# Kernel tuning notes

Measured on AMD Instinct MI355X. Metric: run time of the kernel, lower is better.

## Reference

```python
import jax, jax.numpy as jnp
import numpy as np

N, G, E, R = 32768, 2048, 1146880, 3
NIN, GIN, F, OUT = 6, 4, 64, 1


def _w(k, fan_in, fan_out):
    return (jax.random.normal(k, (fan_in, fan_out), jnp.float32) / np.sqrt(fan_in)).astype(jnp.float32)


def setup_inputs() -> dict:
    key = jax.random.key(0)
    ks = jax.random.split(key, 20)
    x = jax.random.normal(ks[0], (N, NIN), jnp.float32)
    u = jax.random.normal(ks[1], (G, GIN), jnp.float32)
    batch = jnp.sort(jax.random.randint(ks[2], (N,), 0, G))
    hyperedge_index = jax.random.randint(ks[3], (R, E), 0, N)
    batch_hyper = jnp.sort(jax.random.randint(ks[4], (E,), 0, G))
    inp = {
        "x": x, "u": u, "batch": batch,
        "hyperedge_index": hyperedge_index, "batch_hyper": batch_hyper, "r": R,
        # mlp_x: (NIN+GIN)->F->F->F
        "W1": _w(ks[5], NIN + GIN, F), "b1": jnp.zeros((F,), jnp.float32),
        "W2": _w(ks[6], F, F), "b2": jnp.zeros((F,), jnp.float32),
        "W3": _w(ks[7], F, F), "b3": jnp.zeros((F,), jnp.float32),
        # weighting matrix [F,F]
        "weight": _w(ks[8], F, F),
        # x_hat: 2F->F->F->OUT
        "V1": _w(ks[9], 2 * F, F), "c1": jnp.zeros((F,), jnp.float32),
        "V2": _w(ks[10], F, F), "c2": jnp.zeros((F,), jnp.float32),
        "V3": _w(ks[11], F, OUT), "c3": jnp.zeros((OUT,), jnp.float32),
    }
    return inp


def _segment_softmax(x, idx, num_segments):
    # torch_geometric-style softmax grouped by idx along dim 0, per feature
    seg_max = jax.ops.segment_max(x, idx, num_segments=num_segments)
    ex = jnp.exp(x - seg_max[idx])
    denom = jax.ops.segment_sum(ex, idx, num_segments=num_segments)
    return ex / denom[idx]


def reference(x, u, batch, hyperedge_index, batch_hyper, r,
              W1, b1, W2, b2, W3, b3, weight, V1, c1, V2, c2, V3, c3):
    # mlp_x on [node_feats || global_feats_of_node's_graph]
    h = jnp.concatenate([x, u[batch]], axis=1)            # [N, NIN+GIN]
    h = jnp.maximum(h @ W1 + b1, 0.0)
    h = jnp.maximum(h @ W2 + b2, 0.0)
    h = h @ W3 + b3                                        # [N, F]

    # hyperedge finding: sum the r member-node embeddings of each hyperedge
    x_hyper = jnp.zeros((hyperedge_index.shape[1], h.shape[1]), h.dtype)
    for i in range(hyperedge_index.shape[0]):              # r is small & fixed
        x_hyper = x_hyper + jnp.take(h, hyperedge_index[i], axis=0)  # [E, F]

    # weighting: segment softmax over hyperedges of the same graph
    coef = _segment_softmax(x_hyper, batch_hyper, G)       # [E, F]
    x_hyper_hat = coef * jnp.maximum(x_hyper @ weight, 0.0)

    # x_hat head
    o = jnp.concatenate([x_hyper, x_hyper_hat], axis=1)    # [E, 2F]
    o = jnp.maximum(o @ V1 + c1, 0.0)
    o = jnp.maximum(o @ V2 + c2, 0.0)
    o = jax.nn.sigmoid(o @ V3 + c3)                        # [E, OUT]
    return (o, batch_hyper)
```

## Files before the change

kernel.cpp:

```cpp
#include <hip/hip_runtime.h>
#include <math.h>

typedef short bf16x8 __attribute__((ext_vector_type(8)));
typedef float f32x4  __attribute__((ext_vector_type(4)));
typedef unsigned short u16;
typedef unsigned int   u32;

#define MFMA16 __builtin_amdgcn_mfma_f32_16x16x32_bf16

__device__ __forceinline__ u16 f2b(float x) {
    union { float f; unsigned u; } v; v.f = x;
    unsigned r = v.u + 0x7fffu + ((v.u >> 16) & 1u);
    return (u16)(r >> 16);
}
__device__ __forceinline__ u16 f2bu(float x) {
    union { float f; unsigned u; } v; v.f = x;
    return (u16)((v.u + 0x8000u) >> 16);
}
__device__ __forceinline__ float b2f(u16 h) {
    union { unsigned u; float f; } v; v.u = ((unsigned)h) << 16;
    return v.f;
}
__device__ __forceinline__ float blo(u32 w) {
    union { u32 u; float f; } v; v.u = w << 16; return v.f;
}
__device__ __forceinline__ float bhi(u32 w) {
    union { u32 u; float f; } v; v.u = w & 0xffff0000u; return v.f;
}
__device__ __forceinline__ u32 add3pack(u32 x, u32 y, u32 z) {
    union { float f; u32 u; } lo, hi;
    lo.f = blo(x) + blo(y) + blo(z);
    hi.f = bhi(x) + bhi(y) + bhi(z);
    return __builtin_amdgcn_perm(hi.u + 0x8000u, lo.u + 0x8000u, 0x07060302u);
}
__device__ __forceinline__ u32 pack2(float lo, float hi) {
    union { float f; u32 u; } a, b;
    a.f = lo; b.f = hi;
    return __builtin_amdgcn_perm(b.u + 0x8000u, a.u + 0x8000u, 0x07060302u);
}

#define LOG2E 1.44269504088896340736f

__global__ __launch_bounds__(256) void prep_mlp_kernel(
    const float* __restrict__ x, const float* __restrict__ u,
    const int* __restrict__ batch,
    const float* __restrict__ W1, const float* __restrict__ b1,
    const float* __restrict__ W2, const float* __restrict__ b2,
    const float* __restrict__ W3, const float* __restrict__ b3,
    u16* __restrict__ hb, int N,
    const float* __restrict__ Wg, const float* __restrict__ V1g,
    const float* __restrict__ V2g, u16* __restrict__ SWZ,
    const int* __restrict__ bh, int E, int G, int* __restrict__ seg_start,
    int SB)
{
    const int b = blockIdx.x, tid = threadIdx.x;
    if (b < 32) {
        int idx = b * 256 + tid;
        int k = idx >> 6, n = idx & 63;
        int s1 = (k < 64) ? k : (64 + (((k - 64) & 15) << 2) + ((k - 64) >> 4));
        int off1 = ((s1 >> 5) * 4 + (n >> 4)) * 512 + (n & 15) * 32 + ((s1 >> 3) & 3) * 8 + (s1 & 7);
        SWZ[4096 + off1] = f2b(V1g[idx]);
        if (idx < 4096) {
            int offw = ((k >> 5) * 4 + (n >> 4)) * 512 + (n & 15) * 32 + ((k >> 3) & 3) * 8 + (k & 7);
            SWZ[offw] = f2b(Wg[idx]);
            int s2 = ((k & 15) << 2) + (k >> 4);
            int off2 = ((s2 >> 5) * 4 + (n >> 4)) * 512 + (n & 15) * 32 + ((s2 >> 3) & 3) * 8 + (s2 & 7);
            SWZ[12288 + off2] = f2b(V2g[idx]);
        }
        return;
    }
    if (b < 32 + SB) {
        int g = (b - 32) * 256 + tid;
        if (g > G) return;
        int lo = 0, hi = E;
        while (lo < hi) {
            int mid = (lo + hi) >> 1;
            if (bh[mid] < g) lo = mid + 1; else hi = mid;
        }
        seg_start[g] = lo;
        return;
    }
    __shared__ float inbuf[16][10];
    __shared__ float h1[16][64];
    __shared__ float h2[16][64];
    const int ni = tid >> 6, f = tid & 63;
    const int base = (b - 32 - SB) * 16;
    int nodes[4];
    #pragma unroll
    for (int s = 0; s < 4; ++s) {
        nodes[s] = min(base + s * 4 + ni, N - 1);
        if (f < 6)       inbuf[s * 4 + ni][f] = x[nodes[s] * 6 + f];
        else if (f < 10) inbuf[s * 4 + ni][f] = u[batch[nodes[s]] * 4 + (f - 6)];
    }
    __syncthreads();
    float acc[4];
    #pragma unroll
    for (int s = 0; s < 4; ++s) acc[s] = b1[f];
    #pragma unroll
    for (int k = 0; k < 10; ++k) {
        float w = W1[k * 64 + f];
        #pragma unroll
        for (int s = 0; s < 4; ++s) acc[s] = fmaf(inbuf[s * 4 + ni][k], w, acc[s]);
    }
    #pragma unroll
    for (int s = 0; s < 4; ++s) h1[s * 4 + ni][f] = fmaxf(acc[s], 0.f);
    __syncthreads();
    #pragma unroll
    for (int s = 0; s < 4; ++s) acc[s] = b2[f];
    #pragma unroll
    for (int k4 = 0; k4 < 16; ++k4) {
        float w0 = W2[(k4 * 4 + 0) * 64 + f];
        float w1 = W2[(k4 * 4 + 1) * 64 + f];
        float w2 = W2[(k4 * 4 + 2) * 64 + f];
        float w3 = W2[(k4 * 4 + 3) * 64 + f];
        #pragma unroll
        for (int s = 0; s < 4; ++s) {
            float4 hv = *(const float4*)&h1[s * 4 + ni][k4 * 4];
            acc[s] = fmaf(hv.x, w0, acc[s]);
            acc[s] = fmaf(hv.y, w1, acc[s]);
            acc[s] = fmaf(hv.z, w2, acc[s]);
            acc[s] = fmaf(hv.w, w3, acc[s]);
        }
    }
    #pragma unroll
    for (int s = 0; s < 4; ++s) h2[s * 4 + ni][f] = fmaxf(acc[s], 0.f);
    __syncthreads();
    #pragma unroll
    for (int s = 0; s < 4; ++s) acc[s] = b3[f];
    #pragma unroll
    for (int k4 = 0; k4 < 16; ++k4) {
        float w0 = W3[(k4 * 4 + 0) * 64 + f];
        float w1 = W3[(k4 * 4 + 1) * 64 + f];
        float w2 = W3[(k4 * 4 + 2) * 64 + f];
        float w3 = W3[(k4 * 4 + 3) * 64 + f];
        #pragma unroll
        for (int s = 0; s < 4; ++s) {
            float4 hv = *(const float4*)&h2[s * 4 + ni][k4 * 4];
            acc[s] = fmaf(hv.x, w0, acc[s]);
            acc[s] = fmaf(hv.y, w1, acc[s]);
            acc[s] = fmaf(hv.z, w2, acc[s]);
            acc[s] = fmaf(hv.w, w3, acc[s]);
        }
    }
    #pragma unroll
    for (int s = 0; s < 4; ++s) hb[nodes[s] * 64 + f] = f2b(acc[s]);
}

__global__ __launch_bounds__(256) void gather_stats_kernel(
    const u16* __restrict__ hb, const int* __restrict__ hidx,
    const int* __restrict__ seg_start,
    float* __restrict__ Sinv, float* __restrict__ out, int E)
{
    __shared__ float ps[4][8][8];
    const int tid = threadIdx.x, lane = tid & 63, wid = tid >> 6;
    const int sub = lane >> 3, cl = lane & 7;
    const int g = blockIdx.x;
    const int e0 = seg_start[g], e1 = seg_start[g + 1];
    if (e1 <= e0) return;
    const int e1m1 = e1 - 1;
    const float gf = (float)g;

    for (int e = e0 + tid; e < e1; e += 256) out[E + e] = gf;

    float s[8] = {0.f, 0.f, 0.f, 0.f, 0.f, 0.f, 0.f, 0.f};
    for (int e = e0 + wid * 8 + sub; e < e1; e += 128) {
        #pragma unroll
        for (int j = 0; j < 4; ++j) {
            int ee = e + j * 32;
            int ec = min(ee, e1m1);
            int i0 = hidx[ec], i1 = hidx[E + ec], i2 = hidx[2 * E + ec];
            uint4 A0 = *(const uint4*)(hb + (size_t)i0 * 64 + cl * 8);
            uint4 A1 = *(const uint4*)(hb + (size_t)i1 * 64 + cl * 8);
            uint4 A2 = *(const uint4*)(hb + (size_t)i2 * 64 + cl * 8);
            u32 w0 = add3pack(A0.x, A1.x, A2.x);
            u32 w1 = add3pack(A0.y, A1.y, A2.y);
            u32 w2 = add3pack(A0.z, A1.z, A2.z);
            u32 w3 = add3pack(A0.w, A1.w, A2.w);
            if (ee < e1) {
                s[0] += __expf(blo(w0)); s[1] += __expf(bhi(w0));
                s[2] += __expf(blo(w1)); s[3] += __expf(bhi(w1));
                s[4] += __expf(blo(w2)); s[5] += __expf(bhi(w2));
                s[6] += __expf(blo(w3)); s[7] += __expf(bhi(w3));
            }
        }
    }
    #pragma unroll
    for (int k = 0; k < 8; ++k) {
        s[k] += __shfl_xor(s[k], 8);
        s[k] += __shfl_xor(s[k], 16);
        s[k] += __shfl_xor(s[k], 32);
    }
    if (lane < 8) {
        #pragma unroll
        for (int k = 0; k < 8; ++k) ps[wid][lane][k] = s[k];
    }
    __syncthreads();
    if (tid < 64) {
        int c8 = tid >> 3, cc = tid & 7;
        float S = ps[0][c8][cc] + ps[1][c8][cc] + ps[2][c8][cc] + ps[3][c8][cc];
        Sinv[g * 64 + tid] = 1.f / S;
    }
}

__global__ __launch_bounds__(256, 3) void mfma_seg_kernel(
    const u16* __restrict__ hb, const int* __restrict__ hidx,
    const int* __restrict__ seg_start,
    const u16* __restrict__ SWZ, const float* __restrict__ Sinv,
    const float* __restrict__ c1g, const float* __restrict__ c2g,
    const float* __restrict__ V3g, const float* __restrict__ c3g,
    float* __restrict__ out, int E)
{
    __shared__ u16 SW[16384];
    __shared__ u16 XT_all[4][16 * 64];

    const int tid = threadIdx.x, lane = tid & 63, wid = tid >> 6;
    const int nl = lane & 15, rq = lane >> 4;
    const int g = blockIdx.x;
    const int e0 = seg_start[g], e1 = seg_start[g + 1];
    const int L = e1 - e0;
    if (L <= 0) return;
    const int e1m1 = e1 - 1;

    {
        const uint4* src = (const uint4*)SWZ;
        uint4* dst = (uint4*)SW;
        for (int i = tid; i < 2048; i += 256) dst[i] = src[i];
    }
    __syncthreads();
    const u16* WB  = SW;
    const u16* V1B = SW + 4096;
    const u16* V2B = SW + 12288;

    bf16x8 I0, I1;
    #pragma unroll
    for (int j = 0; j < 8; ++j) {
        I0[j] = (rq * 8 + j == nl)      ? (short)0x3F80 : (short)0;
        I1[j] = (rq * 8 + j == nl + 16) ? (short)0x3F80 : (short)0;
    }

    float l2d[4], c1v[4], c2v[4], v3v[4];
    #pragma unroll
    for (int nt = 0; nt < 4; ++nt) {
        int col = nt * 16 + nl;
        l2d[nt] = __log2f(Sinv[g * 64 + col]);
        c1v[nt] = c1g[col];
        c2v[nt] = c2g[col];
        v3v[nt] = V3g[col];
    }
    const float c3s = c3g[0];
    u16* XT = XT_all[wid];
    const f32x4 zf = {0.f, 0.f, 0.f, 0.f};

    const int xw_swz = rq << 4;
    const int xr_base = nl * 64;
    const int xr_swz  = (nl & 12) << 2;
    const int xr0 = xr_base + ((rq * 8) ^ xr_swz);
    const int xr1 = xr_base + ((rq * 8 + 32) ^ xr_swz);

    auto loadA = [&](int tt, bf16x8& A0, bf16x8& A1) {
        const int ec = min(e0 + tt * 16 + nl, e1m1);
        const int i0 = hidx[ec], i1 = hidx[E + ec], i2 = hidx[2 * E + ec];
        const u16* r0 = hb + (size_t)i0 * 64 + rq * 8;
        const u16* r1 = hb + (size_t)i1 * 64 + rq * 8;
        const u16* r2 = hb + (size_t)i2 * 64 + rq * 8;
        uint4 B0 = *(const uint4*)(r0), C0 = *(const uint4*)(r0 + 32);
        uint4 B1 = *(const uint4*)(r1), C1 = *(const uint4*)(r1 + 32);
        uint4 B2 = *(const uint4*)(r2), C2 = *(const uint4*)(r2 + 32);
        union { uint4 q; bf16x8 h; } u0, u1v;
        u0.q.x  = add3pack(B0.x, B1.x, B2.x);
        u0.q.y  = add3pack(B0.y, B1.y, B2.y);
        u0.q.z  = add3pack(B0.z, B1.z, B2.z);
        u0.q.w  = add3pack(B0.w, B1.w, B2.w);
        u1v.q.x = add3pack(C0.x, C1.x, C2.x);
        u1v.q.y = add3pack(C0.y, C1.y, C2.y);
        u1v.q.z = add3pack(C0.z, C1.z, C2.z);
        u1v.q.w = add3pack(C0.w, C1.w, C2.w);
        A0 = u0.h;
        A1 = u1v.h;
    };

    int t = wid;
    bf16x8 p0 = {}, p1 = {};
    if (t * 16 < L) loadA(t, p0, p1);

    for (; t * 16 < L; t += 8) {
        const int eB1 = e0 + t * 16;
        const int eB2 = eB1 + 64;

        bf16x8 a0 = p0, a1 = p1;
        bf16x8 a2, a3;
        loadA(t + 4, a2, a3);
        if ((t + 8) * 16 < L) loadA(t + 8, p0, p1);

        f32x4 xc1[4], xc2[4];
        xc1[0] = MFMA16(a0, I0, zf, 0, 0, 0);
        xc1[1] = MFMA16(a0, I1, zf, 0, 0, 0);
        xc1[2] = MFMA16(a1, I0, zf, 0, 0, 0);
        xc1[3] = MFMA16(a1, I1, zf, 0, 0, 0);
        xc2[0] = MFMA16(a2, I0, zf, 0, 0, 0);
        xc2[1] = MFMA16(a2, I1, zf, 0, 0, 0);
        xc2[2] = MFMA16(a3, I0, zf, 0, 0, 0);
        xc2[3] = MFMA16(a3, I1, zf, 0, 0, 0);

        f32x4 acc1[4] = {zf, zf, zf, zf}, acc2t[4] = {zf, zf, zf, zf};
        #pragma unroll
        for (int nt = 0; nt < 4; ++nt) {
            bf16x8 b0 = *(const bf16x8*)(WB + (0 * 4 + nt) * 512 + nl * 32 + rq * 8);
            acc1[nt]  = MFMA16(a0, b0, acc1[nt], 0, 0, 0);
            acc2t[nt] = MFMA16(a2, b0, acc2t[nt], 0, 0, 0);
            bf16x8 b1 = *(const bf16x8*)(WB + (1 * 4 + nt) * 512 + nl * 32 + rq * 8);
            acc1[nt]  = MFMA16(a1, b1, acc1[nt], 0, 0, 0);
            acc2t[nt] = MFMA16(a3, b1, acc2t[nt], 0, 0, 0);
        }
        #pragma unroll
        for (int r = 0; r < 4; ++r) {
            float v0 = __builtin_amdgcn_exp2f(fmaf(xc1[0][r], LOG2E, l2d[0])) * fmaxf(acc1[0][r], 0.f);
            float v1 = __builtin_amdgcn_exp2f(fmaf(xc1[1][r], LOG2E, l2d[1])) * fmaxf(acc1[1][r], 0.f);
            float v2 = __builtin_amdgcn_exp2f(fmaf(xc1[2][r], LOG2E, l2d[2])) * fmaxf(acc1[2][r], 0.f);
            float v3 = __builtin_amdgcn_exp2f(fmaf(xc1[3][r], LOG2E, l2d[3])) * fmaxf(acc1[3][r], 0.f);
            uint2 w; w.x = pack2(v0, v1); w.y = pack2(v2, v3);
            *(uint2*)(XT + (rq * 4 + r) * 64 + ((nl * 4) ^ xw_swz)) = w;
        }
        bf16x8 x2a = *(const bf16x8*)(XT + xr0);
        bf16x8 x3a = *(const bf16x8*)(XT + xr1);
        #pragma unroll
        for (int r = 0; r < 4; ++r) {
            float v0 = __builtin_amdgcn_exp2f(fmaf(xc2[0][r], LOG2E, l2d[0])) * fmaxf(acc2t[0][r], 0.f);
            float v1 = __builtin_amdgcn_exp2f(fmaf(xc2[1][r], LOG2E, l2d[1])) * fmaxf(acc2t[1][r], 0.f);
            float v2 = __builtin_amdgcn_exp2f(fmaf(xc2[2][r], LOG2E, l2d[2])) * fmaxf(acc2t[2][r], 0.f);
            float v3 = __builtin_amdgcn_exp2f(fmaf(xc2[3][r], LOG2E, l2d[3])) * fmaxf(acc2t[3][r], 0.f);
            uint2 w; w.x = pack2(v0, v1); w.y = pack2(v2, v3);
            *(uint2*)(XT + (rq * 4 + r) * 64 + ((nl * 4) ^ xw_swz)) = w;
        }
        bf16x8 x2b = *(const bf16x8*)(XT + xr0);
        bf16x8 x3b = *(const bf16x8*)(XT + xr1);

        f32x4 va[4], vb[4];
        #pragma unroll
        for (int nt = 0; nt < 4; ++nt) {
            va[nt][0] = c1v[nt]; va[nt][1] = c1v[nt];
            va[nt][2] = c1v[nt]; va[nt][3] = c1v[nt];
            vb[nt] = va[nt];
        }
        #pragma unroll
        for (int nt = 0; nt < 4; ++nt) {
            bf16x8 b0 = *(const bf16x8*)(V1B + (0 * 4 + nt) * 512 + nl * 32 + rq * 8);
            va[nt] = MFMA16(a0, b0, va[nt], 0, 0, 0);
            vb[nt] = MFMA16(a2, b0, vb[nt], 0, 0, 0);
            bf16x8 b1 = *(const bf16x8*)(V1B + (1 * 4 + nt) * 512 + nl * 32 + rq * 8);
            va[nt] = MFMA16(a1, b1, va[nt], 0, 0, 0);
            vb[nt] = MFMA16(a3, b1, vb[nt], 0, 0, 0);
        }
        #pragma unroll
        for (int nt = 0; nt < 4; ++nt) {
            bf16x8 b2 = *(const bf16x8*)(V1B + (2 * 4 + nt) * 512 + nl * 32 + rq * 8);
            va[nt] = MFMA16(x2a, b2, va[nt], 0, 0, 0);
            vb[nt] = MFMA16(x2b, b2, vb[nt], 0, 0, 0);
            bf16x8 b3 = *(const bf16x8*)(V1B + (3 * 4 + nt) * 512 + nl * 32 + rq * 8);
            va[nt] = MFMA16(x3a, b3, va[nt], 0, 0, 0);
            vb[nt] = MFMA16(x3b, b3, vb[nt], 0, 0, 0);
        }
        #pragma unroll
        for (int r = 0; r < 4; ++r) {
            uint2 w;
            w.x = pack2(fmaxf(va[0][r], 0.f), fmaxf(va[1][r], 0.f));
            w.y = pack2(fmaxf(va[2][r], 0.f), fmaxf(va[3][r], 0.f));
            *(uint2*)(XT + (rq * 4 + r) * 64 + ((nl * 4) ^ xw_swz)) = w;
        }
        bf16x8 o0a = *(const bf16x8*)(XT + xr0);
        bf16x8 o1a = *(const bf16x8*)(XT + xr1);
        #pragma unroll
        for (int r = 0; r < 4; ++r) {
            uint2 w;
            w.x = pack2(fmaxf(vb[0][r], 0.f), fmaxf(vb[1][r], 0.f));
            w.y = pack2(fmaxf(vb[2][r], 0.f), fmaxf(vb[3][r], 0.f));
            *(uint2*)(XT + (rq * 4 + r) * 64 + ((nl * 4) ^ xw_swz)) = w;
        }
        bf16x8 o0b = *(const bf16x8*)(XT + xr0);
        bf16x8 o1b = *(const bf16x8*)(XT + xr1);

        f32x4 wa[4], wb2[4];
        #pragma unroll
        for (int nt = 0; nt < 4; ++nt) {
            wa[nt][0] = c2v[nt]; wa[nt][1] = c2v[nt];
            wa[nt][2] = c2v[nt]; wa[nt][3] = c2v[nt];
            wb2[nt] = wa[nt];
        }
        #pragma unroll
        for (int nt = 0; nt < 4; ++nt) {
            bf16x8 b0 = *(const bf16x8*)(V2B + (0 * 4 + nt) * 512 + nl * 32 + rq * 8);
            wa[nt]  = MFMA16(o0a, b0, wa[nt], 0, 0, 0);
            wb2[nt] = MFMA16(o0b, b0, wb2[nt], 0, 0, 0);
            bf16x8 b1 = *(const bf16x8*)(V2B + (1 * 4 + nt) * 512 + nl * 32 + rq * 8);
            wa[nt]  = MFMA16(o1a, b1, wa[nt], 0, 0, 0);
            wb2[nt] = MFMA16(o1b, b1, wb2[nt], 0, 0, 0);
        }

        float sra[4], srb[4];
        #pragma unroll
        for (int r = 0; r < 4; ++r) {
            float u1 = 0.f, u2 = 0.f;
            #pragma unroll
            for (int nt = 0; nt < 4; ++nt) {
                u1 = fmaf(fmaxf(wa[nt][r],  0.f), v3v[nt], u1);
                u2 = fmaf(fmaxf(wb2[nt][r], 0.f), v3v[nt], u2);
            }
            u1 += __shfl_xor(u1, 1); u2 += __shfl_xor(u2, 1);
            u1 += __shfl_xor(u1, 2); u2 += __shfl_xor(u2, 2);
            u1 += __shfl_xor(u1, 4); u2 += __shfl_xor(u2, 4);
            u1 += __shfl_xor(u1, 8); u2 += __shfl_xor(u2, 8);
            sra[r] = 1.f / (1.f + __expf(-(u1 + c3s)));
            srb[r] = 1.f / (1.f + __expf(-(u2 + c3s)));
        }
        if (nl == 0) {
            const int ra = eB1 + rq * 4;
            if (ra + 3 < e1) {
                *(float4*)(out + ra) = make_float4(sra[0], sra[1], sra[2], sra[3]);
            } else {
                #pragma unroll
                for (int r = 0; r < 4; ++r)
                    if (ra + r < e1) out[ra + r] = sra[r];
            }
            const int rb = eB2 + rq * 4;
            if (rb + 3 < e1) {
                *(float4*)(out + rb) = make_float4(srb[0], srb[1], srb[2], srb[3]);
            } else {
                #pragma unroll
                for (int r = 0; r < 4; ++r)
                    if (rb + r < e1) out[rb + r] = srb[r];
            }
        }
    }
}

extern "C" void kernel_launch(void* const* d_in, const int* in_sizes, int n_in,
                              void* d_out, int out_size, void* d_ws, size_t ws_size,
                              hipStream_t stream) {
    const float* x     = (const float*)d_in[0];
    const float* u     = (const float*)d_in[1];
    const int*   batch = (const int*)  d_in[2];
    const int*   hidx  = (const int*)  d_in[3];
    const int*   bh    = (const int*)  d_in[4];
    const float* W1 = (const float*)d_in[6];
    const float* b1 = (const float*)d_in[7];
    const float* W2 = (const float*)d_in[8];
    const float* b2 = (const float*)d_in[9];
    const float* W3 = (const float*)d_in[10];
    const float* b3 = (const float*)d_in[11];
    const float* Wg = (const float*)d_in[12];
    const float* V1 = (const float*)d_in[13];
    const float* c1 = (const float*)d_in[14];
    const float* V2 = (const float*)d_in[15];
    const float* c2 = (const float*)d_in[16];
    const float* V3 = (const float*)d_in[17];
    const float* c3 = (const float*)d_in[18];

    const int N = in_sizes[0] / 6;
    const int G = in_sizes[1] / 4;
    const int E = in_sizes[4];

    char* ws = (char*)d_ws;
    size_t off = 0;
    u16* hb = (u16*)(ws + off);            off += (size_t)N * 64 * 2;
    int* seg_start = (int*)(ws + off);     off += ((size_t)G + 1) * 4;
    off = (off + 255) & ~(size_t)255;
    u16* SWZ = (u16*)(ws + off);           off += 16384 * 2;
    float* Sinv = (float*)(ws + off);      off += (size_t)G * 64 * 4;
    float* out = (float*)d_out;

    const int SB = (G + 256) / 256;
    const int NB = (N + 15) / 16;
    prep_mlp_kernel<<<32 + SB + NB, 256, 0, stream>>>(
        x, u, batch, W1, b1, W2, b2, W3, b3, hb, N,
        Wg, V1, V2, SWZ, bh, E, G, seg_start, SB);
    gather_stats_kernel<<<G, 256, 0, stream>>>(hb, hidx, seg_start, Sinv, out, E);
    mfma_seg_kernel<<<G, 256, 0, stream>>>(
        hb, hidx, seg_start, SWZ, Sinv, c1, c2, V3, c3, out, E);
}
```

Before: 238.2 us.

## Fuse stats and MFMA segment kernels, caching gathered hyperedge sums in LDS

Merges the softmax-denominator kernel and the MFMA head kernel into one per-graph kernel. During the stats pass, the 3-way gathered hyperedge sums are stored in a swizzled LDS buffer, up to 768 edges per graph. The MFMA phase then reads them from LDS instead of re-gathering from global memory. This removes a kernel launch, the Sinv round-trip and the second gather. In exchange, LDS use rises to about 137KB per block and occupancy drops to one block per CU.

```diff
diff --git a/kernel.cpp b/kernel.cpp
--- a/kernel.cpp
+++ b/kernel.cpp
@@ -40,6 +40,7 @@
 }
 
 #define LOG2E 1.44269504088896340736f
+#define LMAX  768
 
 __global__ __launch_bounds__(256) void prep_mlp_kernel(
     const float* __restrict__ x, const float* __restrict__ u,
@@ -146,87 +147,85 @@
     for (int s = 0; s < 4; ++s) hb[nodes[s] * 64 + f] = f2b(acc[s]);
 }
 
-__global__ __launch_bounds__(256) void gather_stats_kernel(
+__global__ __launch_bounds__(256, 1) void fused_seg_kernel(
     const u16* __restrict__ hb, const int* __restrict__ hidx,
-    const int* __restrict__ seg_start,
-    float* __restrict__ Sinv, float* __restrict__ out, int E)
-{
-    __shared__ float ps[4][8][8];
-    const int tid = threadIdx.x, lane = tid & 63, wid = tid >> 6;
-    const int sub = lane >> 3, cl = lane & 7;
-    const int g = blockIdx.x;
-    const int e0 = seg_start[g], e1 = seg_start[g + 1];
-    if (e1 <= e0) return;
-    const int e1m1 = e1 - 1;
-    const float gf = (float)g;
-
-    for (int e = e0 + tid; e < e1; e += 256) out[E + e] = gf;
-
-    float s[8] = {0.f, 0.f, 0.f, 0.f, 0.f, 0.f, 0.f, 0.f};
-    for (int e = e0 + wid * 8 + sub; e < e1; e += 128) {
-        #pragma unroll
-        for (int j = 0; j < 4; ++j) {
-            int ee = e + j * 32;
-            int ec = min(ee, e1m1);
-            int i0 = hidx[ec], i1 = hidx[E + ec], i2 = hidx[2 * E + ec];
-            uint4 A0 = *(const uint4*)(hb + (size_t)i0 * 64 + cl * 8);
-            uint4 A1 = *(const uint4*)(hb + (size_t)i1 * 64 + cl * 8);
-            uint4 A2 = *(const uint4*)(hb + (size_t)i2 * 64 + cl * 8);
-            u32 w0 = add3pack(A0.x, A1.x, A2.x);
-            u32 w1 = add3pack(A0.y, A1.y, A2.y);
-            u32 w2 = add3pack(A0.z, A1.z, A2.z);
-            u32 w3 = add3pack(A0.w, A1.w, A2.w);
-            if (ee < e1) {
-                s[0] += __expf(blo(w0)); s[1] += __expf(bhi(w0));
-                s[2] += __expf(blo(w1)); s[3] += __expf(bhi(w1));
-                s[4] += __expf(blo(w2)); s[5] += __expf(bhi(w2));
-                s[6] += __expf(blo(w3)); s[7] += __expf(bhi(w3));
-            }
-        }
-    }
-    #pragma unroll
-    for (int k = 0; k < 8; ++k) {
-        s[k] += __shfl_xor(s[k], 8);
-        s[k] += __shfl_xor(s[k], 16);
-        s[k] += __shfl_xor(s[k], 32);
-    }
-    if (lane < 8) {
-        #pragma unroll
-        for (int k = 0; k < 8; ++k) ps[wid][lane][k] = s[k];
-    }
-    __syncthreads();
-    if (tid < 64) {
-        int c8 = tid >> 3, cc = tid & 7;
-        float S = ps[0][c8][cc] + ps[1][c8][cc] + ps[2][c8][cc] + ps[3][c8][cc];
-        Sinv[g * 64 + tid] = 1.f / S;
-    }
-}
-
-__global__ __launch_bounds__(256, 3) void mfma_seg_kernel(
-    const u16* __restrict__ hb, const int* __restrict__ hidx,
-    const int* __restrict__ seg_start,
-    const u16* __restrict__ SWZ, const float* __restrict__ Sinv,
+    const int* __restrict__ seg_start, const u16* __restrict__ SWZ,
     const float* __restrict__ c1g, const float* __restrict__ c2g,
     const float* __restrict__ V3g, const float* __restrict__ c3g,
     float* __restrict__ out, int E)
 {
     __shared__ u16 SW[16384];
+    __shared__ u16 XC[LMAX * 64];
     __shared__ u16 XT_all[4][16 * 64];
+    __shared__ float ps[4][8][8];
+    __shared__ float Sf[64];
 
     const int tid = threadIdx.x, lane = tid & 63, wid = tid >> 6;
-    const int nl = lane & 15, rq = lane >> 4;
     const int g = blockIdx.x;
     const int e0 = seg_start[g], e1 = seg_start[g + 1];
     const int L = e1 - e0;
     if (L <= 0) return;
     const int e1m1 = e1 - 1;
+    const bool inLds = (L <= LMAX);
 
     {
         const uint4* src = (const uint4*)SWZ;
         uint4* dst = (uint4*)SW;
         for (int i = tid; i < 2048; i += 256) dst[i] = src[i];
     }
-    __syncthreads();
+
+    {
+        const int sub = lane >> 3, cl = lane & 7;
+        const float gf = (float)g;
+        for (int e = e0 + tid; e < e1; e += 256) out[E + e] = gf;
+
+        float s[8] = {0.f, 0.f, 0.f, 0.f, 0.f, 0.f, 0.f, 0.f};
+        for (int e = e0 + wid * 8 + sub; e < e1; e += 128) {
+            #pragma unroll
+            for (int j = 0; j < 4; ++j) {
+                int ee = e + j * 32;
+                int ec = min(ee, e1m1);
+                int i0 = hidx[ec], i1 = hidx[E + ec], i2 = hidx[2 * E + ec];
+                uint4 A0 = *(const uint4*)(hb + (size_t)i0 * 64 + cl * 8);
+                uint4 A1 = *(const uint4*)(hb + (size_t)i1 * 64 + cl * 8);
+                uint4 A2 = *(const uint4*)(hb + (size_t)i2 * 64 + cl * 8);
+                u32 w0 = add3pack(A0.x, A1.x, A2.x);
+                u32 w1 = add3pack(A0.y, A1.y, A2.y);
+                u32 w2 = add3pack(A0.z, A1.z, A2.z);
+                u32 w3 = add3pack(A0.w, A1.w, A2.w);
+                if (ee < e1) {
+                    if (inLds) {
+                        int le = ee - e0;
+                        uint4 W; W.x = w0; W.y = w1; W.z = w2; W.w = w3;
+                        *(uint4*)(XC + le * 64 + ((cl * 8) ^ ((le & 7) << 3))) = W;
+                    }
+                    s[0] += __expf(blo(w0)); s[1] += __expf(bhi(w0));
+                    s[2] += __expf(blo(w1)); s[3] += __expf(bhi(w1));
+                    s[4] += __expf(blo(w2)); s[5] += __expf(bhi(w2));
+                    s[6] += __expf(blo(w3)); s[7] += __expf(bhi(w3));
+                }
+            }
+        }
+        #pragma unroll
+        for (int k = 0; k < 8; ++k) {
+            s[k] += __shfl_xor(s[k], 8);
+            s[k] += __shfl_xor(s[k], 16);
+            s[k] += __shfl_xor(s[k], 32);
+        }
+        if (lane < 8) {
+            #pragma unroll
+            for (int k = 0; k < 8; ++k) ps[wid][lane][k] = s[k];
+        }
+        __syncthreads();
+        if (tid < 64) {
+            int c8 = tid >> 3, cc = tid & 7;
+            float S = ps[0][c8][cc] + ps[1][c8][cc] + ps[2][c8][cc] + ps[3][c8][cc];
+            Sf[tid] = 1.f / S;
+        }
+        __syncthreads();
+    }
+
+    const int nl = lane & 15, rq = lane >> 4;
     const u16* WB  = SW;
     const u16* V1B = SW + 4096;
     const u16* V2B = SW + 12288;
@@ -242,7 +241,7 @@
     #pragma unroll
     for (int nt = 0; nt < 4; ++nt) {
         int col = nt * 16 + nl;
-        l2d[nt] = __log2f(Sinv[g * 64 + col]);
+        l2d[nt] = __log2f(Sf[col]);
         c1v[nt] = c1g[col];
         c2v[nt] = c2g[col];
         v3v[nt] = V3g[col];
@@ -258,25 +257,33 @@
     const int xr1 = xr_base + ((rq * 8 + 32) ^ xr_swz);
 
     auto loadA = [&](int tt, bf16x8& A0, bf16x8& A1) {
-        const int ec = min(e0 + tt * 16 + nl, e1m1);
-        const int i0 = hidx[ec], i1 = hidx[E + ec], i2 = hidx[2 * E + ec];
-        const u16* r0 = hb + (size_t)i0 * 64 + rq * 8;
-        const u16* r1 = hb + (size_t)i1 * 64 + rq * 8;
-        const u16* r2 = hb + (size_t)i2 * 64 + rq * 8;
-        uint4 B0 = *(const uint4*)(r0), C0 = *(const uint4*)(r0 + 32);
-        uint4 B1 = *(const uint4*)(r1), C1 = *(const uint4*)(r1 + 32);
-        uint4 B2 = *(const uint4*)(r2), C2 = *(const uint4*)(r2 + 32);
-        union { uint4 q; bf16x8 h; } u0, u1v;
-        u0.q.x  = add3pack(B0.x, B1.x, B2.x);
-        u0.q.y  = add3pack(B0.y, B1.y, B2.y);
-        u0.q.z  = add3pack(B0.z, B1.z, B2.z);
-        u0.q.w  = add3pack(B0.w, B1.w, B2.w);
-        u1v.q.x = add3pack(C0.x, C1.x, C2.x);
-        u1v.q.y = add3pack(C0.y, C1.y, C2.y);
-        u1v.q.z = add3pack(C0.z, C1.z, C2.z);
-        u1v.q.w = add3pack(C0.w, C1.w, C2.w);
-        A0 = u0.h;
-        A1 = u1v.h;
+        if (inLds) {
+            const int le = min(tt * 16 + nl, L - 1);
+            const u16* p = XC + le * 64;
+            const int sw = (le & 7) << 3;
+            A0 = *(const bf16x8*)(p + ((rq * 8) ^ sw));
+            A1 = *(const bf16x8*)(p + ((rq * 8 + 32) ^ sw));
+        } else {
+            const int ec = min(e0 + tt * 16 + nl, e1m1);
+            const int i0 = hidx[ec], i1 = hidx[E + ec], i2 = hidx[2 * E + ec];
+            const u16* r0 = hb + (size_t)i0 * 64 + rq * 8;
+            const u16* r1 = hb + (size_t)i1 * 64 + rq * 8;
+            const u16* r2 = hb + (size_t)i2 * 64 + rq * 8;
+            uint4 B0 = *(const uint4*)(r0), C0 = *(const uint4*)(r0 + 32);
+            uint4 B1 = *(const uint4*)(r1), C1 = *(const uint4*)(r1 + 32);
+            uint4 B2 = *(const uint4*)(r2), C2 = *(const uint4*)(r2 + 32);
+            union { uint4 q; bf16x8 h; } u0, u1v;
+            u0.q.x  = add3pack(B0.x, B1.x, B2.x);
+            u0.q.y  = add3pack(B0.y, B1.y, B2.y);
+            u0.q.z  = add3pack(B0.z, B1.z, B2.z);
+            u0.q.w  = add3pack(B0.w, B1.w, B2.w);
+            u1v.q.x = add3pack(C0.x, C1.x, C2.x);
+            u1v.q.y = add3pack(C0.y, C1.y, C2.y);
+            u1v.q.z = add3pack(C0.z, C1.z, C2.z);
+            u1v.q.w = add3pack(C0.w, C1.w, C2.w);
+            A0 = u0.h;
+            A1 = u1v.h;
+        }
     };
 
     int t = wid;
@@ -465,7 +472,6 @@
     int* seg_start = (int*)(ws + off);     off += ((size_t)G + 1) * 4;
     off = (off + 255) & ~(size_t)255;
     u16* SWZ = (u16*)(ws + off);           off += 16384 * 2;
-    float* Sinv = (float*)(ws + off);      off += (size_t)G * 64 * 4;
     float* out = (float*)d_out;
 
     const int SB = (G + 256) / 256;
@@ -473,7 +479,6 @@
     prep_mlp_kernel<<<32 + SB + NB, 256, 0, stream>>>(
         x, u, batch, W1, b1, W2, b2, W3, b3, hb, N,
         Wg, V1, V2, SWZ, bh, E, G, seg_start, SB);
-    gather_stats_kernel<<<G, 256, 0, stream>>>(hb, hidx, seg_start, Sinv, out, E);
-    mfma_seg_kernel<<<G, 256, 0, stream>>>(
-        hb, hidx, seg_start, SWZ, Sinv, c1, c2, V3, c3, out, E);
-}
+    fused_seg_kernel<<<G, 256, 0, stream>>>(
+        hb, hidx, seg_start, SWZ, c1, c2, V3, c3, out, E);
+}
```

Measured after the change: 352.6 us. 1.48x slower.
